# Optimization experiments

Measured on AMD Instinct MI355X. Metric: run time of the kernel, lower is better.

## Reference

```python
import jax, jax.numpy as jnp
import numpy as np

B, S, E = 8, 4096, 128
H, O = 64, 64  # attention_hidden_dim, out_dim


def setup_inputs() -> dict:
    key = jax.random.key(0)
    ks = jax.random.split(key, 4)
    x = jax.random.normal(ks[0], (B, S, E), dtype=jnp.float32)
    Wq = jax.random.normal(ks[1], (E, H), dtype=jnp.float32) * (1.0 / np.sqrt(E))
    Wk = jax.random.normal(ks[2], (E, H), dtype=jnp.float32) * (1.0 / np.sqrt(E))
    Wv = jax.random.normal(ks[3], (E, O), dtype=jnp.float32) * (1.0 / np.sqrt(E))
    bq = jnp.zeros((H,), dtype=jnp.float32)
    bk = jnp.zeros((H,), dtype=jnp.float32)
    bv = jnp.zeros((O,), dtype=jnp.float32)
    return {"x": x, "Wq": Wq, "bq": bq, "Wk": Wk, "bk": bk, "Wv": Wv, "bv": bv}


def reference(x, Wq, bq, Wk, bk, Wv, bv):
    # Batched version of the per-sample loop: q = x@Wq+bq, etc.
    q = jnp.einsum("bse,eh->bsh", x, Wq) + bq   # [B,S,H]
    k = jnp.einsum("bse,eh->bsh", x, Wk) + bk   # [B,S,H]
    v = jnp.einsum("bse,eo->bso", x, Wv) + bv   # [B,S,O]
    scores = jnp.einsum("bqh,bkh->bqk", q, k)   # QK^T per sample, [B,S,S]
    attn = jax.nn.softmax(scores, axis=-1)       # softmax over key dim
    out = jnp.einsum("bqk,bko->bqo", attn, v)   # [B,S,O]
    return out
```

## Files before the change

kernel.cpp:

```cpp
#include <hip/hip_runtime.h>
#include <math.h>

#define BB 8
#define SS 4096
#define EE 128
#define HH 64
#define NT 16
#define LOG2E 1.44269504088896f

typedef _Float16 f16;
typedef __attribute__((ext_vector_type(8))) _Float16 f16x8;
typedef __attribute__((ext_vector_type(4))) float f32x4;
typedef __attribute__((ext_vector_type(16))) float f32x16;
typedef __attribute__((ext_vector_type(4))) unsigned int u32x4;

__device__ __forceinline__ unsigned int pk2h(float a, float b) {
    return __builtin_bit_cast(unsigned int, __builtin_amdgcn_cvt_pkrtz(a, b));
}

__device__ __forceinline__ void async_copy16(void* lds, const void* g) {
    __builtin_amdgcn_global_load_lds(
        (const __attribute__((address_space(1))) void*)g,
        (__attribute__((address_space(3))) void*)lds, 16, 0, 0);
}

__device__ __forceinline__ void vm_barrier() {
    asm volatile("s_waitcnt vmcnt(0) lgkmcnt(0)" ::: "memory");
    __builtin_amdgcn_s_barrier();
    __builtin_amdgcn_sched_barrier(0);
}

__global__ __launch_bounds__(256) void wtrans_kernel(
    const float* __restrict__ Wq, const float* __restrict__ Wk,
    const float* __restrict__ Wv, f16* __restrict__ Wt)
{
    const int idx = blockIdx.x * 256 + threadIdx.x;
    if (idx >= 192 * 128) return;
    const int col = idx >> 7, e = idx & 127;
    const float v = (col < 64)  ? Wq[e * 64 + col] * LOG2E
                  : (col < 128) ? Wk[e * 64 + (col - 64)]
                                : Wv[e * 64 + (col - 128)];
    Wt[col * 128 + e] = (f16)v;
}

__global__ __launch_bounds__(256) void qkv_kernel(
    const float* __restrict__ x, const f16* __restrict__ Wt,
    const float* __restrict__ bq, const float* __restrict__ bk,
    const float* __restrict__ bv,
    f16* __restrict__ Q, f16* __restrict__ K, f16* __restrict__ Vt)
{
    __shared__ __align__(16) short xs[64 * EE];
    const int tid = threadIdx.x;
    const long rowbase = (long)blockIdx.x * 64;

    {
        const float4* xg = (const float4*)(x + rowbase * EE);
#pragma unroll
        for (int j = 0; j < 8; ++j) {
            const int eidx = tid * 32 + j * 4;
            const float4 v = xg[eidx >> 2];
            unsigned long long pk =
                (unsigned long long)pk2h(v.x, v.y) |
                ((unsigned long long)pk2h(v.z, v.w) << 32);
            const int row = eidx >> 7;
            const int off = (row * 256 + (eidx & 127) * 2) ^ ((row & 7) << 4);
            *(unsigned long long*)((char*)xs + off) = pk;
        }
    }
    __syncthreads();

    const int lane = tid & 63;
    const int wid  = tid >> 6;
    const int ln15 = lane & 15;
    const int lg   = lane >> 4;

    f16x8 xa[4];
    {
        const int row = wid * 16 + ln15;
        const int swz = (row & 7) << 4;
#pragma unroll
        for (int s = 0; s < 4; ++s)
            xa[s] = *(const f16x8*)((const char*)xs + ((row * 256 + lg * 16 + s * 64) ^ swz));
    }

    f32x4 acc[12];
#pragma unroll
    for (int ct = 0; ct < 12; ++ct) acc[ct] = (f32x4){0.f, 0.f, 0.f, 0.f};

#pragma unroll
    for (int ct = 0; ct < 12; ++ct) {
        const f16* wtp = Wt + (ct * 16 + ln15) * 128 + lg * 8;
#pragma unroll
        for (int s = 0; s < 4; ++s) {
            const f16x8 wb = *(const f16x8*)(wtp + s * 32);
            acc[ct] = __builtin_amdgcn_mfma_f32_16x16x32_f16(xa[s], wb, acc[ct], 0, 0, 0);
        }
    }

    const long grow0 = rowbase + wid * 16 + 4 * lg;
#pragma unroll
    for (int ct = 0; ct < 4; ++ct) {
        const int col = ct * 16 + ln15;
        const float b = bq[col] * LOG2E;
#pragma unroll
        for (int r = 0; r < 4; ++r)
            Q[(grow0 + r) * HH + col] = (f16)(acc[ct][r] + b);
    }
#pragma unroll
    for (int ct = 4; ct < 8; ++ct) {
        const int col = (ct - 4) * 16 + ln15;
        const float b = bk[col];
#pragma unroll
        for (int r = 0; r < 4; ++r)
            K[(grow0 + r) * HH + col] = (f16)(acc[ct][r] + b);
    }
    {
        const long batch = rowbase >> 12;
        const long inrow = (rowbase & 4095) + wid * 16 + 4 * lg;
#pragma unroll
        for (int ct = 8; ct < 12; ++ct) {
            const int o = (ct - 8) * 16 + ln15;
            const float b = bv[o];
            unsigned long long pk =
                (unsigned long long)pk2h(acc[ct][0] + b, acc[ct][1] + b) |
                ((unsigned long long)pk2h(acc[ct][2] + b, acc[ct][3] + b) << 32);
            *(unsigned long long*)(Vt + ((long)batch * HH + o) * SS + inrow) = pk;
        }
    }
}

__global__ __launch_bounds__(256, 4) void flash_kernel(
    const f16* __restrict__ Q, const f16* __restrict__ K,
    const f16* __restrict__ Vt, f16* __restrict__ Onorm,
    float* __restrict__ lse)
{
    __shared__ __align__(16) short k_s[2][64 * HH];
    __shared__ __align__(16) short v_s[2][64 * HH];

    const int tid  = threadIdx.x;
    const int lane = tid & 63;
    const int wid  = tid >> 6;
    const int q31  = lane & 31;
    const int h5   = lane >> 5;
    const int batch = blockIdx.x & 7;
    const int split = (blockIdx.x >> 3) & 3;
    const int qblk  = blockIdx.x >> 5;
    const int k0base = split * (SS / 4);

    f16x8 qf[4];
    {
        const long qrow = (long)batch * SS + qblk * 128 + wid * 32 + q31;
        const f16* qp = Q + qrow * HH + 8 * h5;
        qf[0] = *(const f16x8*)(qp);
        qf[1] = *(const f16x8*)(qp + 16);
        qf[2] = *(const f16x8*)(qp + 32);
        qf[3] = *(const f16x8*)(qp + 48);
    }

    f32x16 oacc0 = {0.f,0.f,0.f,0.f,0.f,0.f,0.f,0.f,0.f,0.f,0.f,0.f,0.f,0.f,0.f,0.f};
    f32x16 oacc1 = oacc0;
    float m = -1e30f, l = 0.f;

    const int crow = lane >> 3;
    const int ccs  = ((lane & 7) * 16) ^ (crow << 4);
    const int row0 = wid * 16 + crow;
    const char* kgb = (const char*)(K + ((long)batch * SS + k0base) * HH);
    const char* vgb = (const char*)(Vt + (long)batch * HH * SS);
    const long koff = (long)row0 * 128 + ccs;
    const long voff = (long)row0 * (SS * 2) + k0base * 2 + ccs;

    auto issue = [&](int t, int b) __attribute__((always_inline)) {
        char* kl = (char*)k_s[b] + wid * 2048;
        char* vl = (char*)v_s[b] + wid * 2048;
        const char* kg = kgb + (long)t * (64 * 128) + koff;
        const char* vg = vgb + (long)t * 128 + voff;
        async_copy16(kl,        kg);
        async_copy16(kl + 1024, kg + 1024);
        async_copy16(vl,        vg);
        async_copy16(vl + 1024, vg + 8 * (SS * 2));
    };

    auto compute = [&](int cur) __attribute__((always_inline)) {
        const char* ks = (const char*)k_s[cur];
        const char* vs = (const char*)v_s[cur];

        f32x16 s0 = {0.f,0.f,0.f,0.f,0.f,0.f,0.f,0.f,0.f,0.f,0.f,0.f,0.f,0.f,0.f,0.f};
        f32x16 s1 = s0;
        __builtin_amdgcn_s_setprio(1);
#pragma unroll
        for (int step = 0; step < 4; ++step) {
            const int cb = step * 32 + 16 * h5;
            const int r0 = q31;
            const f16x8 ka0 = *(const f16x8*)(ks + ((r0 * 128 + cb) ^ ((r0 & 7) << 4)));
            s0 = __builtin_amdgcn_mfma_f32_32x32x16_f16(ka0, qf[step], s0, 0, 0, 0);
            const int r1 = q31 + 32;
            const f16x8 ka1 = *(const f16x8*)(ks + ((r1 * 128 + cb) ^ ((r1 & 7) << 4)));
            s1 = __builtin_amdgcn_mfma_f32_32x32x16_f16(ka1, qf[step], s1, 0, 0, 0);
        }
        __builtin_amdgcn_s_setprio(0);

        float tm = s0[0];
#pragma unroll
        for (int i = 1; i < 16; ++i) tm = fmaxf(tm, s0[i]);
#pragma unroll
        for (int i = 0; i < 16; ++i) tm = fmaxf(tm, s1[i]);
        tm = fmaxf(tm, __shfl_xor(tm, 32));
        if (!__all(tm <= m + 11.5f)) {
            const float mn = fmaxf(m, tm);
            const float alpha = __builtin_amdgcn_exp2f(m - mn);
            l *= alpha;
            oacc0 *= alpha;
            oacc1 *= alpha;
            m = mn;
        }

        unsigned int pk[16];
        float ps = 0.f;
#pragma unroll
        for (int i = 0; i < 8; ++i) {
            const float a = __builtin_amdgcn_exp2f(s0[2 * i] - m);
            const float b = __builtin_amdgcn_exp2f(s0[2 * i + 1] - m);
            ps += a + b;
            pk[i] = pk2h(a, b);
        }
#pragma unroll
        for (int i = 0; i < 8; ++i) {
            const float a = __builtin_amdgcn_exp2f(s1[2 * i] - m);
            const float b = __builtin_amdgcn_exp2f(s1[2 * i + 1] - m);
            ps += a + b;
            pk[8 + i] = pk2h(a, b);
        }
        ps += __shfl_xor(ps, 32);
        l += ps;

        __builtin_amdgcn_s_setprio(1);
#pragma unroll
        for (int mb = 0; mb < 4; ++mb) {
            const u32x4 pw = {pk[4 * mb], pk[4 * mb + 1], pk[4 * mb + 2], pk[4 * mb + 3]};
            const f16x8 pb = __builtin_bit_cast(f16x8, pw);
            const int cb_lo = 32 * mb + 8 * h5;
#pragma unroll
            for (int oh = 0; oh < 2; ++oh) {
                const int row = q31 + 32 * oh;
                const int swz = (row & 7) << 4;
                const uint2 lo = *(const uint2*)(vs + ((row * 128 + cb_lo) ^ swz));
                const uint2 hi = *(const uint2*)(vs + ((row * 128 + cb_lo + 16) ^ swz));
                const u32x4 w = {lo.x, lo.y, hi.x, hi.y};
                const f16x8 va = __builtin_bit_cast(f16x8, w);
                if (oh == 0)
                    oacc0 = __builtin_amdgcn_mfma_f32_32x32x16_f16(va, pb, oacc0, 0, 0, 0);
                else
                    oacc1 = __builtin_amdgcn_mfma_f32_32x32x16_f16(va, pb, oacc1, 0, 0, 0);
            }
        }
        __builtin_amdgcn_s_setprio(0);
    };

    issue(0, 0);
    vm_barrier();

    for (int t = 0; t < NT; t += 2) {
        issue(t + 1, 1);
        compute(0);
        vm_barrier();
        if (t + 2 < NT) issue(t + 2, 0);
        compute(1);
        vm_barrier();
    }

    const float linv = 1.0f / l;
    const long tok = (long)split * (BB * SS) + (long)batch * SS + qblk * 128 + wid * 32 + q31;
    f16* ob = Onorm + tok * HH;
#pragma unroll
    for (int i = 0; i < 16; ++i) {
        const int od = (i & 3) + 8 * (i >> 2) + 4 * h5;
        ob[od]      = (f16)(oacc0[i] * linv);
        ob[od + 32] = (f16)(oacc1[i] * linv);
    }
    if (h5 == 0)
        lse[tok] = m + __builtin_amdgcn_logf(l);
}

__global__ __launch_bounds__(256) void merge_kernel(
    const f16* __restrict__ Onorm, const float* __restrict__ lse,
    float* __restrict__ Out)
{
    const int gid = blockIdx.x * 256 + threadIdx.x;
    const long row = gid >> 3;
    const int c0 = (gid & 7) * 8;
    const long NR = (long)BB * SS;

    float ls[4];
#pragma unroll
    for (int i = 0; i < 4; ++i) ls[i] = lse[i * NR + row];
    const float M = fmaxf(fmaxf(ls[0], ls[1]), fmaxf(ls[2], ls[3]));
    float g[4], denom = 0.f;
#pragma unroll
    for (int i = 0; i < 4; ++i) { g[i] = __builtin_amdgcn_exp2f(ls[i] - M); denom += g[i]; }
    const float inv = 1.0f / denom;

    float acc[8];
#pragma unroll
    for (int j = 0; j < 8; ++j) acc[j] = 0.f;
#pragma unroll
    for (int i = 0; i < 4; ++i) {
        const f16x8 o = *(const f16x8*)(Onorm + (i * NR + row) * HH + c0);
#pragma unroll
        for (int j = 0; j < 8; ++j) acc[j] = fmaf(g[i], (float)o[j], acc[j]);
    }
    float4 r0, r1;
    r0.x = acc[0] * inv; r0.y = acc[1] * inv; r0.z = acc[2] * inv; r0.w = acc[3] * inv;
    r1.x = acc[4] * inv; r1.y = acc[5] * inv; r1.z = acc[6] * inv; r1.w = acc[7] * inv;
    float4* dst = (float4*)(Out + row * HH + c0);
    dst[0] = r0;
    dst[1] = r1;
}

extern "C" void kernel_launch(void* const* d_in, const int* in_sizes, int n_in,
                              void* d_out, int out_size, void* d_ws, size_t ws_size,
                              hipStream_t stream) {
    const float* x  = (const float*)d_in[0];
    const float* Wq = (const float*)d_in[1];
    const float* bq = (const float*)d_in[2];
    const float* Wk = (const float*)d_in[3];
    const float* bk = (const float*)d_in[4];
    const float* Wv = (const float*)d_in[5];
    const float* bv = (const float*)d_in[6];
    float* out = (float*)d_out;

    const size_t NTOK = (size_t)BB * SS;
    f16* Q  = (f16*)d_ws;
    f16* K  = Q + NTOK * HH;
    f16* Vt = K + NTOK * HH;
    f16* Wt = Vt + NTOK * HH;
    f16* Onorm = Wt + 192 * 128;
    float* lse = (float*)(Onorm + 4 * NTOK * HH);

    wtrans_kernel<<<96, 256, 0, stream>>>(Wq, Wk, Wv, Wt);
    qkv_kernel<<<BB * SS / 64, 256, 0, stream>>>(x, Wt, bq, bk, bv, Q, K, Vt);
    flash_kernel<<<BB * 4 * (SS / 128), 256, 0, stream>>>(Q, K, Vt, Onorm, lse);
    merge_kernel<<<BB * SS * 8 / 256, 256, 0, stream>>>(Onorm, lse, out);
}
```

Before: 81.93 us.

## Load x directly into registers and permute Vt layout for 16-byte V reads

The QKV projection kernel now loads x straight from global memory into MFMA operand registers, converting to fp16 in place. This drops the LDS staging buffer and its __syncthreads. The Vt store permutes row positions within each 16-row group so the flash kernel can fetch each V operand with one 16-byte LDS read instead of two 8-byte reads. This relies on the permutation matching the P operand ordering. It also changes global access coalescing for x.

```diff
diff --git a/kernel.cpp b/kernel.cpp
--- a/kernel.cpp
+++ b/kernel.cpp
@@ -49,38 +49,24 @@
     const float* __restrict__ bv,
     f16* __restrict__ Q, f16* __restrict__ K, f16* __restrict__ Vt)
 {
-    __shared__ __align__(16) short xs[64 * EE];
-    const int tid = threadIdx.x;
-    const long rowbase = (long)blockIdx.x * 64;
-
-    {
-        const float4* xg = (const float4*)(x + rowbase * EE);
-#pragma unroll
-        for (int j = 0; j < 8; ++j) {
-            const int eidx = tid * 32 + j * 4;
-            const float4 v = xg[eidx >> 2];
-            unsigned long long pk =
-                (unsigned long long)pk2h(v.x, v.y) |
-                ((unsigned long long)pk2h(v.z, v.w) << 32);
-            const int row = eidx >> 7;
-            const int off = (row * 256 + (eidx & 127) * 2) ^ ((row & 7) << 4);
-            *(unsigned long long*)((char*)xs + off) = pk;
-        }
-    }
-    __syncthreads();
-
+    const int tid  = threadIdx.x;
     const int lane = tid & 63;
     const int wid  = tid >> 6;
     const int ln15 = lane & 15;
     const int lg   = lane >> 4;
+    const long rowbase = (long)blockIdx.x * 64;
 
     f16x8 xa[4];
     {
-        const int row = wid * 16 + ln15;
-        const int swz = (row & 7) << 4;
-#pragma unroll
-        for (int s = 0; s < 4; ++s)
-            xa[s] = *(const f16x8*)((const char*)xs + ((row * 256 + lg * 16 + s * 64) ^ swz));
+        const float* xp = x + (rowbase + wid * 16 + ln15) * EE + lg * 8;
+#pragma unroll
+        for (int s = 0; s < 4; ++s) {
+            const float4 u = *(const float4*)(xp + s * 32);
+            const float4 v = *(const float4*)(xp + s * 32 + 4);
+            const u32x4 w = {pk2h(u.x, u.y), pk2h(u.z, u.w),
+                             pk2h(v.x, v.y), pk2h(v.z, v.w)};
+            xa[s] = __builtin_bit_cast(f16x8, w);
+        }
     }
 
     f32x4 acc[12];
@@ -116,7 +102,8 @@
     }
     {
         const long batch = rowbase >> 12;
-        const long inrow = (rowbase & 4095) + wid * 16 + 4 * lg;
+        const long inrow0 = (rowbase & 4095) + wid * 16;
+        const long inrowP = inrow0 + 8 * (lg & 1) + 4 * (lg >> 1);
 #pragma unroll
         for (int ct = 8; ct < 12; ++ct) {
             const int o = (ct - 8) * 16 + ln15;
@@ -124,7 +111,7 @@
             unsigned long long pk =
                 (unsigned long long)pk2h(acc[ct][0] + b, acc[ct][1] + b) |
                 ((unsigned long long)pk2h(acc[ct][2] + b, acc[ct][3] + b) << 32);
-            *(unsigned long long*)(Vt + ((long)batch * HH + o) * SS + inrow) = pk;
+            *(unsigned long long*)(Vt + ((long)batch * HH + o) * SS + inrowP) = pk;
         }
     }
 }
@@ -238,15 +225,11 @@
         for (int mb = 0; mb < 4; ++mb) {
             const u32x4 pw = {pk[4 * mb], pk[4 * mb + 1], pk[4 * mb + 2], pk[4 * mb + 3]};
             const f16x8 pb = __builtin_bit_cast(f16x8, pw);
-            const int cb_lo = 32 * mb + 8 * h5;
+            const int cb = 32 * mb + 16 * h5;
 #pragma unroll
             for (int oh = 0; oh < 2; ++oh) {
                 const int row = q31 + 32 * oh;
-                const int swz = (row & 7) << 4;
-                const uint2 lo = *(const uint2*)(vs + ((row * 128 + cb_lo) ^ swz));
-                const uint2 hi = *(const uint2*)(vs + ((row * 128 + cb_lo + 16) ^ swz));
-                const u32x4 w = {lo.x, lo.y, hi.x, hi.y};
-                const f16x8 va = __builtin_bit_cast(f16x8, w);
+                const f16x8 va = *(const f16x8*)(vs + ((row * 128 + cb) ^ ((row & 7) << 4)));
                 if (oh == 0)
                     oacc0 = __builtin_amdgcn_mfma_f32_32x32x16_f16(va, pb, oacc0, 0, 0, 0);
                 else
```

Result: faster. 78.11 us (-4.7%).
